# Optimization experiments

Measured on AMD Instinct MI355X. Metric: run time of the kernel, lower is better.

## Reference

```python
import jax, jax.numpy as jnp
import numpy as np
from jax import lax

B, S, T = 64, 50, 50
U, E = 1024, 256
VI, VT = 12000, 16000
BOS = 1


def _gru_step(h, x, Wx, Wh, b):
    # Keras GRU v2 (reset_after=True): b[0]=input bias, b[1]=recurrent bias
    gi = x @ Wx + b[0]          # [B, 3U]
    gh = h @ Wh + b[1]          # [B, 3U]
    iz, ir, ih = jnp.split(gi, 3, axis=-1)
    hz, hr, hh = jnp.split(gh, 3, axis=-1)
    z = jax.nn.sigmoid(iz + hz)
    r = jax.nn.sigmoid(ir + hr)
    hcand = jnp.tanh(ih + r * hh)
    return z * h + (1.0 - z) * hcand


def setup_inputs() -> dict:
    key = jax.random.key(0)
    ks = jax.random.split(key, 20)
    f = lambda k, shp: (jax.random.normal(k, shp, dtype=jnp.float32) * 0.05)
    inp = jax.random.randint(ks[0], (B, S), 0, VI)
    targ = jax.random.randint(ks[1], (B, T), 0, VT)
    targ = targ.at[:, 0].set(BOS)  # <bos> first token (teacher forcing input)
    return {
        'inp': inp,
        'targ': targ,
        'enc_hidden': jnp.zeros((B, U), jnp.float32),
        'enc_emb': f(ks[2], (VI, E)),
        'enc_Wx': f(ks[3], (E, 3 * U)),
        'enc_Wh': f(ks[4], (U, 3 * U)),
        'enc_b': jnp.zeros((2, 3 * U), jnp.float32),
        'W1': f(ks[5], (U, U)), 'b1': jnp.zeros((U,), jnp.float32),
        'W2': f(ks[6], (U, U)), 'b2': jnp.zeros((U,), jnp.float32),
        'V': f(ks[7], (U, 1)), 'bV': jnp.zeros((1,), jnp.float32),
        'dec_emb': f(ks[8], (VT, E)),
        'dec_Wx': f(ks[9], (U + E, 3 * U)),
        'dec_Wh': f(ks[10], (U, 3 * U)),
        'dec_b': jnp.zeros((2, 3 * U), jnp.float32),
        'fc_W': f(ks[11], (U, VT)), 'fc_b': jnp.zeros((VT,), jnp.float32),
    }


def reference(inp, targ, enc_hidden, enc_emb, enc_Wx, enc_Wh, enc_b,
              W1, b1, W2, b2, V, bV,
              dec_emb, dec_Wx, dec_Wh, dec_b, fc_W, fc_b):
    # ----- encoder GRU over source -----
    xe = enc_emb[inp]                             # [B,S,E]
    def enc_step(h, xt):
        h2 = _gru_step(h, xt, enc_Wx, enc_Wh, enc_b)
        return h2, h2
    h_last, outs = lax.scan(enc_step, enc_hidden, xe.transpose(1, 0, 2))
    enc_out = outs.transpose(1, 0, 2)             # [B,S,U]

    # ----- teacher-forcing decode -----
    keys = enc_out @ W2 + b2                      # W2(values), precomputed [B,S,U]
    dec_in_emb = dec_emb[targ[:, :-1]]            # [B,T-1,E] (col 0 is <bos>)
    targets = targ[:, 1:]                         # [B,T-1]

    def dec_step(dh, inps):
        x_emb, yt = inps                          # [B,E], [B]
        # Bahdanau attention on dec_hidden
        s = jnp.tanh((dh @ W1 + b1)[:, None, :] + keys)   # [B,S,U]
        score = jnp.einsum('bsu,uo->bso', s, V) + bV      # [B,S,1]
        attn = jax.nn.softmax(score, axis=1)
        ctx = jnp.sum(attn * enc_out, axis=1)             # [B,U]
        x = jnp.concatenate([ctx, x_emb], axis=-1)        # [B,U+E]
        # original code calls gru(x) with NO initial state -> zero h_prev
        h_new = _gru_step(jnp.zeros_like(dh), x, dec_Wx, dec_Wh, dec_b)
        logits = h_new @ fc_W + fc_b                      # [B,VT]
        logp = jax.nn.log_softmax(logits, axis=-1)
        nll = -jnp.take_along_axis(logp, yt[:, None], axis=1)[:, 0]
        mask = (yt != 0).astype(nll.dtype)
        return h_new, jnp.mean(nll * mask)

    _, losses = lax.scan(dec_step, h_last,
                         (dec_in_emb.transpose(1, 0, 2), targets.T))
    return jnp.sum(losses)
```

## Files before the change

kernel.cpp:

```cpp
#include <hip/hip_runtime.h>
#include <cstdint>
#include <cstddef>

#define BB 64
#define SS 50
#define TT 50
#define TD 49
#define UU 1024
#define EE 256
#define VT 16000
#define G3 3072
#define MPAD 3200

using short8 = __attribute__((ext_vector_type(8))) short;
using short4v = __attribute__((ext_vector_type(4))) short;
using uint4v = __attribute__((ext_vector_type(4))) unsigned int;
using f32x4  = __attribute__((ext_vector_type(4))) float;

__device__ __forceinline__ short f2bf(float f) {
    uint32_t u = __float_as_uint(f);
    uint32_t r = (u + 0x7fffu + ((u >> 16) & 1u)) >> 16;
    return (short)r;
}
__device__ __forceinline__ float bf2f(short s) {
    return __uint_as_float(((uint32_t)(uint16_t)s) << 16);
}
__device__ __forceinline__ float sigm(float x) { return 1.0f / (1.0f + __expf(-x)); }
__device__ __forceinline__ float ftanh(float x) {
    float xc = fminf(fmaxf(x, -8.0f), 8.0f);
    float e = __expf(2.0f * xc);
    return (e - 1.0f) / (e + 1.0f);
}

__device__ __forceinline__ void vstore_bf(short* p, float v) { *(volatile short*)p = f2bf(v); }

__device__ __forceinline__ void gbar(int* flags, int* go, int t) {
    asm volatile("s_waitcnt vmcnt(0)" ::: "memory");
    __syncthreads();
    if (blockIdx.x == 0) {
        if (threadIdx.x < 64) {
            if (threadIdx.x == 0)
                __hip_atomic_store(&flags[0], t, __ATOMIC_RELAXED, __HIP_MEMORY_SCOPE_AGENT);
            int v;
            do {
                v = __hip_atomic_load(&flags[threadIdx.x], __ATOMIC_RELAXED, __HIP_MEMORY_SCOPE_AGENT);
            } while (__ballot(v >= t) != ~0ull);
            if (threadIdx.x == 0)
                __hip_atomic_store(go, t, __ATOMIC_RELAXED, __HIP_MEMORY_SCOPE_AGENT);
        }
    } else {
        if (threadIdx.x == 0) {
            __hip_atomic_store(&flags[blockIdx.x], t, __ATOMIC_RELAXED, __HIP_MEMORY_SCOPE_AGENT);
            while (__hip_atomic_load(go, __ATOMIC_RELAXED, __HIP_MEMORY_SCOPE_AGENT) < t)
                __builtin_amdgcn_s_sleep(1);
        }
    }
    __syncthreads();
    asm volatile("" ::: "memory");
}

typedef __attribute__((address_space(3))) void lds_vp;
typedef __attribute__((address_space(1))) void gl_vp;
__device__ __forceinline__ void gload16(void* lds, const void* g) {
    __builtin_amdgcn_global_load_lds((const gl_vp*)(uintptr_t)g,
                                     (lds_vp*)(uint32_t)(uintptr_t)lds,
                                     16, 0, 0);
}
__device__ __forceinline__ f32x4 mfma16(short8 a, short8 b, f32x4 c) {
    return __builtin_amdgcn_mfma_f32_16x16x32_bf16(a, b, c, 0, 0, 0);
}

template<int BM, int BN, int WM, int WN, bool OUT_BF16, int REMAP>
__global__ __launch_bounds__(256) void gemm_bf16(
    const short* __restrict__ A, const short* __restrict__ Bt,
    const float* __restrict__ bias, void* __restrict__ C, int N, int K,
    int lda, int ldb)
{
    constexpr int BK = 32;
    __shared__ __attribute__((aligned(16))) short As[BM * BK];
    __shared__ __attribute__((aligned(16))) short Bs[BN * BK];

    const int tid  = threadIdx.x;
    const int wave = tid >> 6;
    const int lane = tid & 63;
    const int l15  = lane & 15;
    const int quad = lane >> 4;
    const int wm = wave >> 1, wn = wave & 1;
    const int n0 = blockIdx.x * BN;
    const int m0 = blockIdx.y * BM;

    f32x4 acc[WM / 16][WN / 16];
    #pragma unroll
    for (int i = 0; i < WM / 16; ++i)
        #pragma unroll
        for (int j = 0; j < WN / 16; ++j)
            acc[i][j] = (f32x4)0.0f;

    for (int k0 = 0; k0 < K; k0 += BK) {
        #pragma unroll
        for (int it = 0; it < BM / 64; ++it) {
            int e = (it * 256 + tid) * 8;
            int row = e >> 5, col = e & 31;
            gload16(As + (it * 256 + wave * 64) * 8,
                    A + (size_t)(m0 + row) * lda + k0 + col);
        }
        #pragma unroll
        for (int it = 0; it < BN / 64; ++it) {
            int e = (it * 256 + tid) * 8;
            int row = e >> 5, col = e & 31;
            gload16(Bs + (it * 256 + wave * 64) * 8,
                    Bt + (size_t)(n0 + row) * ldb + k0 + col);
        }
        __syncthreads();
        short8 af[WM / 16], bfr[WN / 16];
        #pragma unroll
        for (int i = 0; i < WM / 16; ++i)
            af[i] = *(const short8*)(As + (wm * WM + i * 16 + l15) * BK + quad * 8);
        #pragma unroll
        for (int j = 0; j < WN / 16; ++j)
            bfr[j] = *(const short8*)(Bs + (wn * WN + j * 16 + l15) * BK + quad * 8);
        #pragma unroll
        for (int i = 0; i < WM / 16; ++i)
            #pragma unroll
            for (int j = 0; j < WN / 16; ++j)
                acc[i][j] = mfma16(af[i], bfr[j], acc[i][j]);
        __syncthreads();
    }

    #pragma unroll
    for (int i = 0; i < WM / 16; ++i) {
        #pragma unroll
        for (int j = 0; j < WN / 16; ++j) {
            int row = m0 + wm * WM + i * 16 + quad * 4;
            int col = n0 + wn * WN + j * 16 + l15;
            float bia = bias ? bias[col] : 0.0f;
            #pragma unroll
            for (int r = 0; r < 4; ++r) {
                size_t off;
                if (REMAP == 1)
                    off = ((size_t)((row + r) & 63) * SS + ((row + r) >> 6)) * N + col;
                else if (REMAP == 2)
                    off = (((size_t)((row + r) & 63) * SS + ((row + r) >> 6)) * UU
                           + (col & 1023)) * 4 + (col >> 10);
                else
                    off = (size_t)(row + r) * N + col;
                float v = acc[i][j][r] + bia;
                if (OUT_BF16) ((short*)C)[off] = f2bf(v);
                else          ((float*)C)[off] = v;
            }
        }
    }
}

__global__ __launch_bounds__(256) void transpose_bf(
    const float* __restrict__ in, short* __restrict__ out, int ldin, int ldout)
{
    __shared__ float tile[64][65];
    int n0 = blockIdx.x * 64, k0 = blockIdx.y * 64;
    int c = threadIdx.x & 63, rr = threadIdx.x >> 6;
    #pragma unroll 4
    for (int i = 0; i < 16; ++i) {
        int row = rr * 16 + i;
        tile[row][c] = in[(size_t)(k0 + row) * ldin + n0 + c];
    }
    __syncthreads();
    #pragma unroll 4
    for (int i = 0; i < 16; ++i) {
        int row = rr * 16 + i;
        out[(size_t)(n0 + row) * ldout + k0 + c] = f2bf(tile[c][row]);
    }
}

__global__ __launch_bounds__(256) void transpose_pack(
    const float* __restrict__ W, short* __restrict__ Wp, int N, int K)
{
    int lane = threadIdx.x & 63;
    int it = blockIdx.x * 4 + (threadIdx.x >> 6);
    int nt = blockIdx.y;
    int KI = K >> 5;
    int kb = it * 32 + (lane >> 4) * 8;
    int n  = nt * 16 + (lane & 15);
    short8 v;
    #pragma unroll
    for (int e = 0; e < 8; ++e)
        v[e] = f2bf(W[(size_t)(kb + e) * N + n]);
    *(short8*)(Wp + (((size_t)nt * KI + it) * 64 + lane) * 8) = v;
}

__global__ __launch_bounds__(256) void prep_gather(
    const int* __restrict__ inp, const int* __restrict__ targ,
    const float* __restrict__ enc_emb, const float* __restrict__ dec_emb,
    const float* __restrict__ enc_h0,
    short* __restrict__ Ae, short* __restrict__ Ad,
    short* __restrict__ H_bf, short* __restrict__ h0_bf,
    float* __restrict__ out, int* __restrict__ bar)
{
    int blk = blockIdx.x, tid = threadIdx.x;
    if (blk < MPAD) {
        int s = blk >> 6, b = blk & 63;
        int row = inp[b * SS + s];
        Ae[(size_t)blk * EE + tid] = f2bf(enc_emb[(size_t)row * EE + tid]);
    } else if (blk < 2 * MPAD) {
        int m = blk - MPAD;
        if (m < TD * BB) {
            int t = m >> 6, b = m & 63;
            int row = targ[b * TT + t];
            Ad[(size_t)m * EE + tid] = f2bf(dec_emb[(size_t)row * EE + tid]);
        } else {
            Ad[(size_t)m * EE + tid] = 0;
        }
    } else {
        int r = blk - 2 * MPAD;
        for (int u = tid; u < UU; u += 256) {
            H_bf[(size_t)(TD * BB + r) * UU + u] = 0;
            h0_bf[(size_t)r * UU + u] = f2bf(enc_h0[(size_t)r * UU + u]);
        }
        if (r == 0) {
            bar[tid] = 0;
            if (tid == 0) out[0] = 0.0f;
        }
    }
}

__global__ __launch_bounds__(1024) void enc_scan(
    const short* __restrict__ h0, const short* __restrict__ Whp,
    const short* __restrict__ gi, const float* __restrict__ bias2,
    short* __restrict__ eout, int* __restrict__ bar)
{
    const int j    = blockIdx.x;
    const int tid  = threadIdx.x;
    const int lane = tid & 63;
    const int l15  = lane & 15;
    const int quad = lane >> 4;
    const int wave = tid >> 6;
    const int bg   = wave & 3;
    const int kq   = wave >> 2;
    const int u    = j * 16 + l15;

    __shared__ f32x4 red[4][3][4][64];
    int* flags = bar;     int* go = bar + 64;

    const short* Bp0 = Whp + ((((size_t)(0 * 64 + j)) * 32 + kq * 8) * 64 + lane) * 8;
    const short* Bp1 = Whp + ((((size_t)(1 * 64 + j)) * 32 + kq * 8) * 64 + lane) * 8;
    const short* Bp2 = Whp + ((((size_t)(2 * 64 + j)) * 32 + kq * 8) * 64 + lane) * 8;
    const float bz = bias2[u], br = bias2[UU + u], bh = bias2[2 * UU + u];

    for (int t = 0; t < SS; ++t) {
        const short* A = t ? eout + (size_t)(t - 1) * BB * UU : h0;
        const short* Arow = A + (size_t)(bg * 16 + l15) * UU + kq * 256 + quad * 8;
        short8 af[8];
        #pragma unroll
        for (int i = 0; i < 8; ++i) af[i] = *(const short8*)(Arow + i * 32);
        f32x4 a0 = (f32x4)0.0f, a1 = (f32x4)0.0f, a2 = (f32x4)0.0f;
        #pragma unroll
        for (int i = 0; i < 8; ++i) {
            a0 = mfma16(af[i], *(const short8*)(Bp0 + i * 512), a0);
            a1 = mfma16(af[i], *(const short8*)(Bp1 + i * 512), a1);
            a2 = mfma16(af[i], *(const short8*)(Bp2 + i * 512), a2);
        }
        red[kq][0][bg][lane] = a0;
        red[kq][1][bg][lane] = a1;
        red[kq][2][bg][lane] = a2;
        __syncthreads();
        if (kq == 0) {
            f32x4 s0 = red[0][0][bg][lane] + red[1][0][bg][lane] + red[2][0][bg][lane] + red[3][0][bg][lane];
            f32x4 s1 = red[0][1][bg][lane] + red[1][1][bg][lane] + red[2][1][bg][lane] + red[3][1][bg][lane];
            f32x4 s2 = red[0][2][bg][lane] + red[1][2][bg][lane] + red[2][2][bg][lane] + red[3][2][bg][lane];
            const short* git = gi + (size_t)t * BB * G3;
            float hv[4];
            #pragma unroll
            for (int r = 0; r < 4; ++r) {
                int b = bg * 16 + quad * 4 + r;
                hv[r] = bf2f(A[(size_t)b * UU + u]);
            }
            #pragma unroll
            for (int r = 0; r < 4; ++r) {
                int b = bg * 16 + quad * 4 + r;
                const short* gb = git + (size_t)b * G3;
                float iz = bf2f(gb[u]), ir = bf2f(gb[UU + u]), ih = bf2f(gb[2 * UU + u]);
                float z  = sigm(iz + s0[r] + bz);
                float rr = sigm(ir + s1[r] + br);
                float hc = ftanh(ih + rr * (s2[r] + bh));
                vstore_bf(eout + (size_t)t * BB * UU + (size_t)b * UU + u,
                          z * hv[r] + (1.0f - z) * hc);
            }
        }
        if (t != SS - 1) gbar(flags, go, t + 1);
    }
}

__global__ __launch_bounds__(1024) void dec_scan(
    const short* __restrict__ eout, const short* __restrict__ W1p,
    const float* __restrict__ b1, const short* __restrict__ keyp,
    const float* __restrict__ Vw, const float* __restrict__ bV,
    const short* __restrict__ Pp4, const short* __restrict__ xg,
    const float* __restrict__ db1, short* __restrict__ q_t,
    short* __restrict__ Hbf, int* __restrict__ bar)
{
    const int j    = blockIdx.x;
    const int tid  = threadIdx.x;
    const int lane = tid & 63;
    const int l15  = lane & 15;
    const int quad = lane >> 4;
    const int wave = tid >> 6;
    const int bg   = wave & 3;
    const int kq   = wave >> 2;
    const int u    = j * 16 + l15;

    __shared__ f32x4 redq[4][4][64];
    __shared__ float sc[64];
    __shared__ float attnw[64];
    int* flags = bar + 128;  int* go = bar + 192;

    const short* BpQ = W1p + (((size_t)j * 32 + kq * 8) * 64 + lane) * 8;
    const float b1v = b1[u];
    const float bV0 = bV[0];

    float Vl[16];
    #pragma unroll
    for (int e = 0; e < 16; e += 4)
        *(float4*)&Vl[e] = *(const float4*)(Vw + lane * 16 + e);

    const float dz3 = db1[tid], dr3 = db1[UU + tid], dh3 = db1[2 * UU + tid];
    const short* Pb = Pp4 + (size_t)j * SS * UU * 4;

    for (int t = 0; t < TD; ++t) {
        const short* dh = t ? Hbf + (size_t)(t - 1) * BB * UU
                            : eout + (size_t)(SS - 1) * BB * UU;
        short* qt = q_t + (size_t)t * BB * UU;
        {
            const short* Arow = dh + (size_t)(bg * 16 + l15) * UU + kq * 256 + quad * 8;
            short8 af[8];
            #pragma unroll
            for (int i = 0; i < 8; ++i) af[i] = *(const short8*)(Arow + i * 32);
            f32x4 aq = (f32x4)0.0f;
            #pragma unroll
            for (int i = 0; i < 8; ++i)
                aq = mfma16(af[i], *(const short8*)(BpQ + i * 512), aq);
            redq[kq][bg][lane] = aq;
        }
        __syncthreads();
        if (kq == 0) {
            f32x4 s = redq[0][bg][lane] + redq[1][bg][lane] + redq[2][bg][lane] + redq[3][bg][lane];
            #pragma unroll
            for (int r = 0; r < 4; ++r)
                vstore_bf(qt + (size_t)(bg * 16 + quad * 4 + r) * UU + u, s[r] + b1v);
        }
        gbar(flags, go, 2 * t + 1);
        {
            const int b = j;
            float ql[16];
            {
                short8 q0 = *(const short8*)(qt + (size_t)b * UU + lane * 16);
                short8 q1 = *(const short8*)(qt + (size_t)b * UU + lane * 16 + 8);
                #pragma unroll
                for (int e = 0; e < 8; ++e) { ql[e] = bf2f(q0[e]); ql[8 + e] = bf2f(q1[e]); }
            }
            for (int s = wave; s < SS; s += 16) {
                const short* kp = keyp + ((size_t)b * SS + s) * UU + lane * 16;
                short8 k0 = *(const short8*)kp;
                short8 k1 = *(const short8*)(kp + 8);
                float p = 0.0f;
                #pragma unroll
                for (int e = 0; e < 8; ++e) p += Vl[e] * ftanh(ql[e] + bf2f(k0[e]));
                #pragma unroll
                for (int e = 0; e < 8; ++e) p += Vl[8 + e] * ftanh(ql[8 + e] + bf2f(k1[e]));
                #pragma unroll
                for (int off = 32; off; off >>= 1) p += __shfl_down(p, off);
                if (lane == 0) sc[s] = p + bV0;
            }
            __syncthreads();
            if (wave == 0) {
                float v = (lane < SS) ? sc[lane] : -1e30f;
                float m = v;
                #pragma unroll
                for (int off = 32; off; off >>= 1) m = fmaxf(m, __shfl_down(m, off));
                m = __shfl(m, 0);
                float e = (lane < SS) ? __expf(v - m) : 0.0f;
                float ss = e;
                #pragma unroll
                for (int off = 32; off; off >>= 1) ss += __shfl_down(ss, off);
                ss = __shfl(ss, 0);
                if (lane < SS) attnw[lane] = e / ss;
            }
            __syncthreads();
            const short* xb = xg + ((size_t)t * BB + b) * G3;
            float g0 = bf2f(xb[tid]);
            float g1 = bf2f(xb[UU + tid]);
            float g2 = bf2f(xb[2 * UU + tid]);
            const short* Pu = Pb + (size_t)tid * 4;
            #pragma unroll 10
            for (int s = 0; s < SS; ++s) {
                float w = attnw[s];
                short4v pv = *(const short4v*)(Pu + (size_t)s * UU * 4);
                g0 += w * bf2f(pv[0]);
                g1 += w * bf2f(pv[1]);
                g2 += w * bf2f(pv[2]);
            }
            float z  = sigm(g0 + dz3);
            float rr = sigm(g1 + dr3);
            float hc = ftanh(g2 + rr * dh3);
            vstore_bf(Hbf + ((size_t)t * BB + b) * UU + tid, (1.0f - z) * hc);
        }
        if (t != TD - 1) gbar(flags, go, 2 * t + 2);
    }
}

__global__ __launch_bounds__(256) void loss_kernel(
    const float* __restrict__ logits, const int* __restrict__ targ,
    int rows0, float* __restrict__ out)
{
    int gr = rows0 + blockIdx.x;
    int t = gr >> 6;
    if (t >= TD) return;
    int b = gr & 63;
    const float* lp = logits + (size_t)blockIdx.x * VT;
    int tid = threadIdx.x;
    __shared__ float redm[4], reds[4];

    float m = -INFINITY;
    for (int v = tid; v < VT; v += 256) m = fmaxf(m, lp[v]);
    #pragma unroll
    for (int off = 32; off; off >>= 1) m = fmaxf(m, __shfl_down(m, off));
    if ((tid & 63) == 0) redm[tid >> 6] = m;
    __syncthreads();
    float mm = fmaxf(fmaxf(redm[0], redm[1]), fmaxf(redm[2], redm[3]));

    float ssum = 0.0f;
    for (int v = tid; v < VT; v += 256) ssum += expf(lp[v] - mm);
    #pragma unroll
    for (int off = 32; off; off >>= 1) ssum += __shfl_down(ssum, off);
    if ((tid & 63) == 0) reds[tid >> 6] = ssum;
    __syncthreads();
    if (tid == 0) {
        float tot = reds[0] + reds[1] + reds[2] + reds[3];
        int y = targ[b * TT + t + 1];
        float nll = mm + logf(tot) - lp[y];
        if (y != 0) atomicAdd(out, nll * (1.0f / (float)BB));
    }
}

extern "C" void kernel_launch(void* const* d_in, const int* in_sizes, int n_in,
                              void* d_out, int out_size, void* d_ws, size_t ws_size,
                              hipStream_t stream)
{
    (void)in_sizes; (void)n_in; (void)out_size;
    const int*   inp      = (const int*)  d_in[0];
    const int*   targ     = (const int*)  d_in[1];
    const float* enc_h0   = (const float*)d_in[2];
    const float* enc_emb  = (const float*)d_in[3];
    const float* enc_Wx   = (const float*)d_in[4];
    const float* enc_Wh   = (const float*)d_in[5];
    const float* enc_b    = (const float*)d_in[6];
    const float* W1       = (const float*)d_in[7];
    const float* b1       = (const float*)d_in[8];
    const float* W2       = (const float*)d_in[9];
    const float* b2       = (const float*)d_in[10];
    const float* Vw       = (const float*)d_in[11];
    const float* bV       = (const float*)d_in[12];
    const float* dec_emb  = (const float*)d_in[13];
    const float* dec_Wx   = (const float*)d_in[14];
    const float* dec_b    = (const float*)d_in[16];
    const float* fc_W     = (const float*)d_in[17];
    const float* fc_b     = (const float*)d_in[18];
    float* out = (float*)d_out;

    char* p = (char*)d_ws;
    auto alloc = [&](size_t bytes) {
        char* r = (char*)(((uintptr_t)p + 255) & ~(uintptr_t)255);
        p = r + bytes;
        return r;
    };
    short* encWxt  = (short*)alloc((size_t)G3 * EE * 2);
    short* W2t     = (short*)alloc((size_t)UU * UU * 2);
    short* dWxt_c  = (short*)alloc((size_t)G3 * UU * 2);
    short* dWxt_e  = (short*)alloc((size_t)G3 * EE * 2);
    short* fcWt    = (short*)alloc((size_t)VT * UU * 2);
    short* encWhp  = (short*)alloc((size_t)G3 * UU * 2);
    short* W1p     = (short*)alloc((size_t)UU * UU * 2);
    short* Ae      = (short*)alloc((size_t)MPAD * EE * 2);
    short* Ad      = (short*)alloc((size_t)MPAD * EE * 2);
    short* enc_gi  = (short*)alloc((size_t)MPAD * G3 * 2);
    short* xemb_gi = (short*)alloc((size_t)MPAD * G3 * 2);
    short* enc_out = (short*)alloc((size_t)MPAD * UU * 2);
    short* keyp    = (short*)alloc((size_t)MPAD * UU * 2);
    short* Pp4     = (short*)alloc((size_t)MPAD * UU * 4 * 2);
    short* H_bf    = (short*)alloc((size_t)MPAD * UU * 2);
    short* h0_bf   = (short*)alloc((size_t)BB * UU * 2);
    short* q_t     = (short*)alloc((size_t)TD * BB * UU * 2);
    int*   bar     = (int*)alloc(256 * 4);

    size_t used = (size_t)(p - (char*)d_ws);
    size_t avail = (ws_size > used) ? ws_size - used : 0;
    int chunkRows = 640;
    while (chunkRows > 128 && (size_t)chunkRows * VT * 4 + 4096 > avail) chunkRows -= 128;
    float* logits = (float*)alloc((size_t)chunkRows * VT * 4);

    transpose_bf<<<dim3(G3/64, EE/64), 256, 0, stream>>>(enc_Wx, encWxt, G3, EE);
    transpose_bf<<<dim3(UU/64, UU/64), 256, 0, stream>>>(W2, W2t, UU, UU);
    transpose_bf<<<dim3(G3/64, UU/64), 256, 0, stream>>>(dec_Wx, dWxt_c, G3, UU);
    transpose_bf<<<dim3(G3/64, EE/64), 256, 0, stream>>>(dec_Wx + (size_t)UU * G3, dWxt_e, G3, EE);
    transpose_bf<<<dim3(VT/64, UU/64), 256, 0, stream>>>(fc_W, fcWt, VT, UU);
    transpose_pack<<<dim3(8, G3/16), 256, 0, stream>>>(enc_Wh, encWhp, G3, UU);
    transpose_pack<<<dim3(8, UU/16), 256, 0, stream>>>(W1, W1p, UU, UU);
    prep_gather<<<2 * MPAD + 64, 256, 0, stream>>>(inp, targ, enc_emb, dec_emb, enc_h0,
                                                   Ae, Ad, H_bf, h0_bf, out, bar);

    gemm_bf16<128,128,64,64,true,0><<<dim3(G3/128, MPAD/128), 256, 0, stream>>>(
        Ae, encWxt, enc_b, enc_gi, G3, EE, EE, EE);
    gemm_bf16<128,128,64,64,true,0><<<dim3(G3/128, MPAD/128), 256, 0, stream>>>(
        Ad, dWxt_e, dec_b, xemb_gi, G3, EE, EE, EE);

    {
        const short* a0 = h0_bf; const short* a1 = encWhp; const short* a2 = enc_gi;
        const float* a3 = enc_b + G3; short* a4 = enc_out; int* a5 = bar;
        void* args[] = {&a0, &a1, &a2, &a3, &a4, &a5};
        hipLaunchCooperativeKernel((void*)enc_scan, dim3(64), dim3(1024), args, 0, stream);
    }

    gemm_bf16<128,128,64,64,true,1><<<dim3(UU/128, MPAD/128), 256, 0, stream>>>(
        enc_out, W2t, b2, keyp, UU, UU, UU, UU);
    gemm_bf16<128,128,64,64,true,2><<<dim3(G3/128, MPAD/128), 256, 0, stream>>>(
        enc_out, dWxt_c, nullptr, Pp4, G3, UU, UU, UU);

    {
        const short* a0 = enc_out; const short* a1 = W1p; const float* a2 = b1;
        const short* a3 = keyp; const float* a4 = Vw; const float* a5 = bV;
        const short* a6 = Pp4; const short* a7 = xemb_gi; const float* a8 = dec_b + G3;
        short* a9 = q_t; short* a10 = H_bf; int* a11 = bar;
        void* args[] = {&a0, &a1, &a2, &a3, &a4, &a5, &a6, &a7, &a8, &a9, &a10, &a11};
        hipLaunchCooperativeKernel((void*)dec_scan, dim3(64), dim3(1024), args, 0, stream);
    }

    for (int rows0 = 0; rows0 < MPAD; rows0 += chunkRows) {
        int rows = MPAD - rows0; if (rows > chunkRows) rows = chunkRows;
        gemm_bf16<128,128,64,64,false,0><<<dim3(VT/128, rows/128), 256, 0, stream>>>(
            H_bf + (size_t)rows0 * UU, fcWt, fc_b, logits, VT, UU, UU, UU);
        loss_kernel<<<rows, 256, 0, stream>>>(logits, targ, rows0, out);
    }
}
```

Baseline: 2.594 ms.

## Overlap output-projection GEMM with decoder scan using extra cooperative blocks

Adds 125 extra blocks to the cooperative decoder-scan launch. Each one waits on the global barrier counter for every decoder step, then computes that step's 64 rows of logits against a packed fc_W slice with MFMA, writing into a full-size logits buffer. This is meant to hide the large vocabulary projection behind the latency-bound recurrent scan instead of running it afterwards as separate chunked GEMMs. It costs a full logits buffer, an extra barrier at the last step, and 189 co-resident 1024-thread blocks, which may not all fit or may slow the scan blocks.

```diff
diff --git a/kernel.cpp b/kernel.cpp
--- a/kernel.cpp
+++ b/kernel.cpp
@@ -295,14 +295,56 @@
     const float* __restrict__ Vw, const float* __restrict__ bV,
     const short* __restrict__ Pp4, const short* __restrict__ xg,
     const float* __restrict__ db1, short* __restrict__ q_t,
-    short* __restrict__ Hbf, int* __restrict__ bar)
-{
-    const int j    = blockIdx.x;
+    short* __restrict__ Hbf, int* __restrict__ bar,
+    const short* __restrict__ fcWp, const float* __restrict__ fc_b,
+    float* __restrict__ logits)
+{
     const int tid  = threadIdx.x;
     const int lane = tid & 63;
     const int l15  = lane & 15;
     const int quad = lane >> 4;
     const int wave = tid >> 6;
+
+    if (blockIdx.x >= 64) {
+        const int w2 = blockIdx.x - 64;
+        if (w2 >= 125 || logits == nullptr) return;
+        const int c0 = w2 * 128;
+        const int wr = wave >> 2;
+        const int wc = wave & 3;
+        int* go = bar + 192;
+        const int nt0 = (c0 >> 4) + wc * 2;
+        const short* Bp0 = fcWp + (((size_t)nt0 * 32) * 64 + lane) * 8;
+        const short* Bp1 = Bp0 + (size_t)32 * 64 * 8;
+        const float bia0 = fc_b[c0 + wc * 32 + l15];
+        const float bia1 = fc_b[c0 + wc * 32 + 16 + l15];
+        for (int rg = 0; rg < TD; ++rg) {
+            if (tid == 0) {
+                while (__hip_atomic_load(go, __ATOMIC_RELAXED, __HIP_MEMORY_SCOPE_AGENT) < 2 * rg + 2)
+                    __builtin_amdgcn_s_sleep(32);
+            }
+            __syncthreads();
+            asm volatile("" ::: "memory");
+            const short* Ar = Hbf + (size_t)rg * BB * UU
+                            + (size_t)(wr * 16 + l15) * UU + quad * 8;
+            f32x4 a0 = (f32x4)0.0f, a1 = (f32x4)0.0f;
+            #pragma unroll 8
+            for (int it = 0; it < 32; ++it) {
+                short8 af = *(const short8*)(Ar + it * 32);
+                a0 = mfma16(af, *(const short8*)(Bp0 + it * 512), a0);
+                a1 = mfma16(af, *(const short8*)(Bp1 + it * 512), a1);
+            }
+            float* lrow = logits + (size_t)(rg * BB + wr * 16 + quad * 4) * VT
+                        + c0 + wc * 32 + l15;
+            #pragma unroll
+            for (int r = 0; r < 4; ++r) {
+                lrow[(size_t)r * VT]      = a0[r] + bia0;
+                lrow[(size_t)r * VT + 16] = a1[r] + bia1;
+            }
+        }
+        return;
+    }
+
+    const int j    = blockIdx.x;
     const int bg   = wave & 3;
     const int kq   = wave >> 2;
     const int u    = j * 16 + l15;
@@ -402,7 +444,7 @@
             float hc = ftanh(g2 + rr * dh3);
             vstore_bf(Hbf + ((size_t)t * BB + b) * UU + tid, (1.0f - z) * hc);
         }
-        if (t != TD - 1) gbar(flags, go, 2 * t + 2);
+        gbar(flags, go, 2 * t + 2);
     }
 }
 
@@ -492,15 +534,29 @@
 
     size_t used = (size_t)(p - (char*)d_ws);
     size_t avail = (ws_size > used) ? ws_size - used : 0;
-    int chunkRows = 640;
-    while (chunkRows > 128 && (size_t)chunkRows * VT * 4 + 4096 > avail) chunkRows -= 128;
-    float* logits = (float*)alloc((size_t)chunkRows * VT * 4);
+    size_t fullNeed = (size_t)VT * UU * 2 + (size_t)TD * BB * VT * 4 + (1u << 20);
+    int fullMode = (avail >= fullNeed) ? 1 : 0;
+
+    short* fcWp = nullptr;
+    float* logits = nullptr;
+    int chunkRows = 0;
+    if (fullMode) {
+        fcWp   = (short*)alloc((size_t)VT * UU * 2);
+        logits = (float*)alloc((size_t)TD * BB * VT * 4);
+    } else {
+        chunkRows = 640;
+        while (chunkRows > 128 && (size_t)chunkRows * VT * 4 + 4096 > avail) chunkRows -= 128;
+        logits = (float*)alloc((size_t)chunkRows * VT * 4);
+    }
 
     transpose_bf<<<dim3(G3/64, EE/64), 256, 0, stream>>>(enc_Wx, encWxt, G3, EE);
     transpose_bf<<<dim3(UU/64, UU/64), 256, 0, stream>>>(W2, W2t, UU, UU);
     transpose_bf<<<dim3(G3/64, UU/64), 256, 0, stream>>>(dec_Wx, dWxt_c, G3, UU);
     transpose_bf<<<dim3(G3/64, EE/64), 256, 0, stream>>>(dec_Wx + (size_t)UU * G3, dWxt_e, G3, EE);
-    transpose_bf<<<dim3(VT/64, UU/64), 256, 0, stream>>>(fc_W, fcWt, VT, UU);
+    if (fullMode)
+        transpose_pack<<<dim3(8, VT/16), 256, 0, stream>>>(fc_W, fcWp, VT, UU);
+    else
+        transpose_bf<<<dim3(VT/64, UU/64), 256, 0, stream>>>(fc_W, fcWt, VT, UU);
     transpose_pack<<<dim3(8, G3/16), 256, 0, stream>>>(enc_Wh, encWhp, G3, UU);
     transpose_pack<<<dim3(8, UU/16), 256, 0, stream>>>(W1, W1p, UU, UU);
     prep_gather<<<2 * MPAD + 64, 256, 0, stream>>>(inp, targ, enc_emb, dec_emb, enc_h0,
@@ -528,14 +584,21 @@
         const short* a3 = keyp; const float* a4 = Vw; const float* a5 = bV;
         const short* a6 = Pp4; const short* a7 = xemb_gi; const float* a8 = dec_b + G3;
         short* a9 = q_t; short* a10 = H_bf; int* a11 = bar;
-        void* args[] = {&a0, &a1, &a2, &a3, &a4, &a5, &a6, &a7, &a8, &a9, &a10, &a11};
-        hipLaunchCooperativeKernel((void*)dec_scan, dim3(64), dim3(1024), args, 0, stream);
-    }
-
-    for (int rows0 = 0; rows0 < MPAD; rows0 += chunkRows) {
-        int rows = MPAD - rows0; if (rows > chunkRows) rows = chunkRows;
-        gemm_bf16<128,128,64,64,false,0><<<dim3(VT/128, rows/128), 256, 0, stream>>>(
-            H_bf + (size_t)rows0 * UU, fcWt, fc_b, logits, VT, UU, UU, UU);
-        loss_kernel<<<rows, 256, 0, stream>>>(logits, targ, rows0, out);
-    }
-}
+        const short* a12 = fcWp; const float* a13 = fc_b; float* a14 = fullMode ? logits : nullptr;
+        void* args[] = {&a0, &a1, &a2, &a3, &a4, &a5, &a6, &a7, &a8, &a9, &a10, &a11,
+                        &a12, &a13, &a14};
+        int grid = fullMode ? (64 + 125) : 64;
+        hipLaunchCooperativeKernel((void*)dec_scan, dim3(grid), dim3(1024), args, 0, stream);
+    }
+
+    if (fullMode) {
+        loss_kernel<<<TD * BB, 256, 0, stream>>>(logits, targ, 0, out);
+    } else {
+        for (int rows0 = 0; rows0 < MPAD; rows0 += chunkRows) {
+            int rows = MPAD - rows0; if (rows > chunkRows) rows = chunkRows;
+            gemm_bf16<128,128,64,64,false,0><<<dim3(VT/128, rows/128), 256, 0, stream>>>(
+                H_bf + (size_t)rows0 * UU, fcWt, fc_b, logits, VT, UU, UU, UU);
+            loss_kernel<<<rows, 256, 0, stream>>>(logits, targ, rows0, out);
+        }
+    }
+}
```

Measured after the change: 2.873 ms. 1.11x slower.

## Make decoder scan per-batch-row blocks, removing grid-wide barriers

Applied to the files above, without the earlier changes.

Each block now owns one batch row and computes the full W1 projection of its own hidden state with MFMA, keeping the hidden state and query in LDS. This removes the two cooperative grid barriers per step and the global round-trip of q_t. The cost is that each block now reads the whole 1024x1024 W1 matrix every step instead of a 1/64 slice, and the matrix-vector product wastes most MFMA lanes (only one row used).

```diff
diff --git a/kernel.cpp b/kernel.cpp
--- a/kernel.cpp
+++ b/kernel.cpp
@@ -289,74 +289,70 @@
     }
 }
 
-__global__ __launch_bounds__(1024) void dec_scan(
+__global__ __launch_bounds__(512) void dec_scan(
     const short* __restrict__ eout, const short* __restrict__ W1p,
     const float* __restrict__ b1, const short* __restrict__ keyp,
     const float* __restrict__ Vw, const float* __restrict__ bV,
     const short* __restrict__ Pp4, const short* __restrict__ xg,
-    const float* __restrict__ db1, short* __restrict__ q_t,
-    short* __restrict__ Hbf, int* __restrict__ bar)
-{
-    const int j    = blockIdx.x;
+    const float* __restrict__ db1, short* __restrict__ Hbf)
+{
+    const int b    = blockIdx.x;
     const int tid  = threadIdx.x;
     const int lane = tid & 63;
     const int l15  = lane & 15;
     const int quad = lane >> 4;
     const int wave = tid >> 6;
-    const int bg   = wave & 3;
-    const int kq   = wave >> 2;
-    const int u    = j * 16 + l15;
-
-    __shared__ f32x4 redq[4][4][64];
+
+    __shared__ __attribute__((aligned(16))) short dh_lds[UU];
+    __shared__ float q_lds[UU];
     __shared__ float sc[64];
     __shared__ float attnw[64];
-    int* flags = bar + 128;  int* go = bar + 192;
-
-    const short* BpQ = W1p + (((size_t)j * 32 + kq * 8) * 64 + lane) * 8;
-    const float b1v = b1[u];
+
+    dh_lds[tid]       = eout[(size_t)(SS - 1) * BB * UU + (size_t)b * UU + tid];
+    dh_lds[tid + 512] = eout[(size_t)(SS - 1) * BB * UU + (size_t)b * UU + tid + 512];
+
     const float bV0 = bV[0];
-
     float Vl[16];
     #pragma unroll
     for (int e = 0; e < 16; e += 4)
         *(float4*)&Vl[e] = *(const float4*)(Vw + lane * 16 + e);
 
-    const float dz3 = db1[tid], dr3 = db1[UU + tid], dh3 = db1[2 * UU + tid];
-    const short* Pb = Pp4 + (size_t)j * SS * UU * 4;
+    const float dz3a = db1[tid],        dr3a = db1[UU + tid],        dh3a = db1[2 * UU + tid];
+    const float dz3b = db1[tid + 512],  dr3b = db1[UU + tid + 512],  dh3b = db1[2 * UU + tid + 512];
+    const short* Pb = Pp4 + (size_t)b * SS * UU * 4;
+
+    const short* Bw = W1p + (size_t)(wave * 8) * 16384 + (size_t)lane * 8;
+    const int u0 = wave * 128 + l15;
+    float b1v[8];
+    #pragma unroll
+    for (int d = 0; d < 8; ++d) b1v[d] = b1[u0 + d * 16];
+
+    __syncthreads();
 
     for (int t = 0; t < TD; ++t) {
-        const short* dh = t ? Hbf + (size_t)(t - 1) * BB * UU
-                            : eout + (size_t)(SS - 1) * BB * UU;
-        short* qt = q_t + (size_t)t * BB * UU;
         {
-            const short* Arow = dh + (size_t)(bg * 16 + l15) * UU + kq * 256 + quad * 8;
-            short8 af[8];
-            #pragma unroll
-            for (int i = 0; i < 8; ++i) af[i] = *(const short8*)(Arow + i * 32);
-            f32x4 aq = (f32x4)0.0f;
-            #pragma unroll
-            for (int i = 0; i < 8; ++i)
-                aq = mfma16(af[i], *(const short8*)(BpQ + i * 512), aq);
-            redq[kq][bg][lane] = aq;
-        }
-        __syncthreads();
-        if (kq == 0) {
-            f32x4 s = redq[0][bg][lane] + redq[1][bg][lane] + redq[2][bg][lane] + redq[3][bg][lane];
-            #pragma unroll
-            for (int r = 0; r < 4; ++r)
-                vstore_bf(qt + (size_t)(bg * 16 + quad * 4 + r) * UU + u, s[r] + b1v);
-        }
-        gbar(flags, go, 2 * t + 1);
+            f32x4 acc[8];
+            #pragma unroll
+            for (int d = 0; d < 8; ++d) acc[d] = (f32x4)0.0f;
+            #pragma unroll
+            for (int it = 0; it < 32; ++it) {
+                short8 af = *(const short8*)(dh_lds + it * 32 + quad * 8);
+                #pragma unroll
+                for (int d = 0; d < 8; ++d)
+                    acc[d] = mfma16(af, *(const short8*)(Bw + d * 16384 + it * 512), acc[d]);
+            }
+            if (quad == 0) {
+                #pragma unroll
+                for (int d = 0; d < 8; ++d)
+                    q_lds[u0 + d * 16] = acc[d][0] + b1v[d];
+            }
+        }
+        __syncthreads();
         {
-            const int b = j;
             float ql[16];
-            {
-                short8 q0 = *(const short8*)(qt + (size_t)b * UU + lane * 16);
-                short8 q1 = *(const short8*)(qt + (size_t)b * UU + lane * 16 + 8);
-                #pragma unroll
-                for (int e = 0; e < 8; ++e) { ql[e] = bf2f(q0[e]); ql[8 + e] = bf2f(q1[e]); }
-            }
-            for (int s = wave; s < SS; s += 16) {
+            #pragma unroll
+            for (int e = 0; e < 16; ++e) ql[e] = q_lds[lane * 16 + e];
+            for (int s = wave; s < SS; s += 8) {
                 const short* kp = keyp + ((size_t)b * SS + s) * UU + lane * 16;
                 short8 k0 = *(const short8*)kp;
                 short8 k1 = *(const short8*)(kp + 8);
@@ -369,40 +365,58 @@
                 for (int off = 32; off; off >>= 1) p += __shfl_down(p, off);
                 if (lane == 0) sc[s] = p + bV0;
             }
-            __syncthreads();
-            if (wave == 0) {
-                float v = (lane < SS) ? sc[lane] : -1e30f;
-                float m = v;
-                #pragma unroll
-                for (int off = 32; off; off >>= 1) m = fmaxf(m, __shfl_down(m, off));
-                m = __shfl(m, 0);
-                float e = (lane < SS) ? __expf(v - m) : 0.0f;
-                float ss = e;
-                #pragma unroll
-                for (int off = 32; off; off >>= 1) ss += __shfl_down(ss, off);
-                ss = __shfl(ss, 0);
-                if (lane < SS) attnw[lane] = e / ss;
-            }
-            __syncthreads();
+        }
+        __syncthreads();
+        if (wave == 0) {
+            float v = (lane < SS) ? sc[lane] : -1e30f;
+            float m = v;
+            #pragma unroll
+            for (int off = 32; off; off >>= 1) m = fmaxf(m, __shfl_down(m, off));
+            m = __shfl(m, 0);
+            float e = (lane < SS) ? __expf(v - m) : 0.0f;
+            float ss = e;
+            #pragma unroll
+            for (int off = 32; off; off >>= 1) ss += __shfl_down(ss, off);
+            ss = __shfl(ss, 0);
+            if (lane < SS) attnw[lane] = e / ss;
+        }
+        __syncthreads();
+        {
             const short* xb = xg + ((size_t)t * BB + b) * G3;
-            float g0 = bf2f(xb[tid]);
-            float g1 = bf2f(xb[UU + tid]);
-            float g2 = bf2f(xb[2 * UU + tid]);
-            const short* Pu = Pb + (size_t)tid * 4;
-            #pragma unroll 10
+            float g0a = bf2f(xb[tid]);
+            float g1a = bf2f(xb[UU + tid]);
+            float g2a = bf2f(xb[2 * UU + tid]);
+            float g0b = bf2f(xb[tid + 512]);
+            float g1b = bf2f(xb[UU + tid + 512]);
+            float g2b = bf2f(xb[2 * UU + tid + 512]);
+            const short* Pua = Pb + (size_t)tid * 4;
+            const short* Pub = Pb + (size_t)(tid + 512) * 4;
+            #pragma unroll 5
             for (int s = 0; s < SS; ++s) {
                 float w = attnw[s];
-                short4v pv = *(const short4v*)(Pu + (size_t)s * UU * 4);
-                g0 += w * bf2f(pv[0]);
-                g1 += w * bf2f(pv[1]);
-                g2 += w * bf2f(pv[2]);
-            }
-            float z  = sigm(g0 + dz3);
-            float rr = sigm(g1 + dr3);
-            float hc = ftanh(g2 + rr * dh3);
-            vstore_bf(Hbf + ((size_t)t * BB + b) * UU + tid, (1.0f - z) * hc);
-        }
-        if (t != TD - 1) gbar(flags, go, 2 * t + 2);
+                short4v pa = *(const short4v*)(Pua + (size_t)s * UU * 4);
+                short4v pb2 = *(const short4v*)(Pub + (size_t)s * UU * 4);
+                g0a += w * bf2f(pa[0]);
+                g1a += w * bf2f(pa[1]);
+                g2a += w * bf2f(pa[2]);
+                g0b += w * bf2f(pb2[0]);
+                g1b += w * bf2f(pb2[1]);
+                g2b += w * bf2f(pb2[2]);
+            }
+            float za  = sigm(g0a + dz3a);
+            float ra  = sigm(g1a + dr3a);
+            float hca = ftanh(g2a + ra * dh3a);
+            float zb  = sigm(g0b + dz3b);
+            float rb  = sigm(g1b + dr3b);
+            float hcb = ftanh(g2b + rb * dh3b);
+            short hba = f2bf((1.0f - za) * hca);
+            short hbb = f2bf((1.0f - zb) * hcb);
+            Hbf[((size_t)t * BB + b) * UU + tid]       = hba;
+            Hbf[((size_t)t * BB + b) * UU + tid + 512] = hbb;
+            dh_lds[tid]       = hba;
+            dh_lds[tid + 512] = hbb;
+        }
+        __syncthreads();
     }
 }
 
@@ -487,7 +501,6 @@
     short* Pp4     = (short*)alloc((size_t)MPAD * UU * 4 * 2);
     short* H_bf    = (short*)alloc((size_t)MPAD * UU * 2);
     short* h0_bf   = (short*)alloc((size_t)BB * UU * 2);
-    short* q_t     = (short*)alloc((size_t)TD * BB * UU * 2);
     int*   bar     = (int*)alloc(256 * 4);
 
     size_t used = (size_t)(p - (char*)d_ws);
@@ -523,14 +536,8 @@
     gemm_bf16<128,128,64,64,true,2><<<dim3(G3/128, MPAD/128), 256, 0, stream>>>(
         enc_out, dWxt_c, nullptr, Pp4, G3, UU, UU, UU);
 
-    {
-        const short* a0 = enc_out; const short* a1 = W1p; const float* a2 = b1;
-        const short* a3 = keyp; const float* a4 = Vw; const float* a5 = bV;
-        const short* a6 = Pp4; const short* a7 = xemb_gi; const float* a8 = dec_b + G3;
-        short* a9 = q_t; short* a10 = H_bf; int* a11 = bar;
-        void* args[] = {&a0, &a1, &a2, &a3, &a4, &a5, &a6, &a7, &a8, &a9, &a10, &a11};
-        hipLaunchCooperativeKernel((void*)dec_scan, dim3(64), dim3(1024), args, 0, stream);
-    }
+    dec_scan<<<dim3(BB), dim3(512), 0, stream>>>(
+        enc_out, W1p, b1, keyp, Vw, bV, Pp4, xemb_gi, dec_b + G3, H_bf);
 
     for (int rows0 = 0; rows0 < MPAD; rows0 += chunkRows) {
         int rows = MPAD - rows0; if (rows > chunkRows) rows = chunkRows;
```

New measurement: 7.191 ms. 177% more time.
